# Optimization experiments

Hardware: AMD Instinct MI355X
Metric: run time of the kernel (lower is better)

## Reference

```python
import jax, jax.numpy as jnp
import numpy as np

G = 4096      # number of graphs in the batch
N = 524288    # total nodes across batch (avg 128 nodes/graph)
H = 128       # hidden_size


def setup_inputs() -> dict:
    key = jax.random.key(0)
    ks = jax.random.split(key, 8)
    s1 = 1.0 / np.sqrt(2 * H)
    s2 = 1.0 / np.sqrt(H)
    return {
        "updated_set": jax.random.normal(ks[0], (G, H), jnp.float32),
        "updated_node": jax.random.normal(ks[1], (N, H), jnp.float32),
        "segment_ids": jnp.sort(jax.random.randint(ks[2], (N,), 0, G, jnp.int32)),
        "Ws1": jax.random.normal(ks[3], (2 * H, H), jnp.float32) * s1,
        "bs1": jnp.zeros((H,), jnp.float32),
        "Ws2": jax.random.normal(ks[4], (H, H), jnp.float32) * s2,
        "bs2": jnp.zeros((H,), jnp.float32),
        "Wn1": jax.random.normal(ks[5], (2 * H, H), jnp.float32) * s1,
        "bn1": jnp.zeros((H,), jnp.float32),
        "Wn2": jax.random.normal(ks[6], (H, H), jnp.float32) * s2,
        "bn2": jnp.zeros((H,), jnp.float32),
    }


def reference(updated_set, updated_node, segment_ids, Ws1, bs1, Ws2, bs2, Wn1, bn1, Wn2, bn2):
    num_graphs = updated_set.shape[0]
    # SumPooling: segment-sum node features per graph -> [G, H]
    nodes_agg = jax.ops.segment_sum(updated_node, segment_ids, num_segments=num_graphs)
    # set update: concat([G,H],[G,H]) -> MLP 2H->H->H with ReLU
    s_in = jnp.concatenate([nodes_agg, updated_set], axis=1)
    s = jax.nn.relu(jax.nn.relu(s_in @ Ws1 + bs1) @ Ws2 + bs2)
    # tile(): broadcast each graph's set state to its nodes = gather by segment id
    n_in = jnp.concatenate([updated_node, s[segment_ids]], axis=1)  # [N, 2H]
    n = jax.nn.relu(jax.nn.relu(n_in @ Wn1 + bn1) @ Wn2 + bn2)
    return s, n
```

## Files before the change

### kernel.cpp

```cpp
#include <hip/hip_runtime.h>

#define NG 4096
#define NN 524288
#define H  128
#define H2 256

typedef __attribute__((ext_vector_type(8))) short bf16x8;
typedef __attribute__((ext_vector_type(4))) float floatx4;
typedef __attribute__((ext_vector_type(2))) unsigned int uint2v;

__device__ __forceinline__ unsigned short bf16r(float f) {
    unsigned int u = __builtin_bit_cast(unsigned int, f);
    u += 0x7fffu + ((u >> 16) & 1u);
    return (unsigned short)(u >> 16);
}
__device__ __forceinline__ unsigned int bf16pk2(float a, float b) {
    return (unsigned int)bf16r(a) | ((unsigned int)bf16r(b) << 16);
}
__device__ __forceinline__ bf16x8 pack8(floatx4 a, floatx4 b) {
    union { unsigned int u[4]; bf16x8 v; } r;
    r.u[0] = bf16pk2(a[0], a[1]);
    r.u[1] = bf16pk2(a[2], a[3]);
    r.u[2] = bf16pk2(b[0], b[1]);
    r.u[3] = bf16pk2(b[2], b[3]);
    return r.v;
}

__global__ __launch_bounds__(128) void seg_sum_kernel(
    const float* __restrict__ node, const int* __restrict__ seg,
    float* __restrict__ agg) {
    const int g = blockIdx.x;
    const int h = threadIdx.x;

    int lo = 0, hi = NN;
    while (lo < hi) { int mid = (lo + hi) >> 1; if (seg[mid] < g) lo = mid + 1; else hi = mid; }
    const int start = lo;
    hi = NN;
    while (lo < hi) { int mid = (lo + hi) >> 1; if (seg[mid] < g + 1) lo = mid + 1; else hi = mid; }
    const int end = lo;

    float a0 = 0.f, a1 = 0.f, a2 = 0.f, a3 = 0.f;
    int i = start;
    for (; i + 3 < end; i += 4) {
        a0 += node[(size_t)i * H + h];
        a1 += node[(size_t)(i + 1) * H + h];
        a2 += node[(size_t)(i + 2) * H + h];
        a3 += node[(size_t)(i + 3) * H + h];
    }
    for (; i < end; ++i) a0 += node[(size_t)i * H + h];
    agg[(size_t)g * H + h] = (a0 + a1) + (a2 + a3);
}

__global__ __launch_bounds__(128) void set_mlp_kernel(
    const float* __restrict__ agg, const float* __restrict__ uset,
    const float* __restrict__ Ws1, const float* __restrict__ bs1,
    const float* __restrict__ Ws2, const float* __restrict__ bs2,
    float* __restrict__ s_out) {
    __shared__ float sin[H2];
    __shared__ float h1[H];
    const int g = blockIdx.x;
    const int j = threadIdx.x;

    sin[j]     = agg[(size_t)g * H + j];
    sin[j + H] = uset[(size_t)g * H + j];
    __syncthreads();

    float acc = bs1[j];
    #pragma unroll 8
    for (int k = 0; k < H2; ++k)
        acc = fmaf(sin[k], Ws1[k * H + j], acc);
    h1[j] = fmaxf(acc, 0.f);
    __syncthreads();

    acc = bs2[j];
    #pragma unroll 8
    for (int k = 0; k < H; ++k)
        acc = fmaf(h1[k], Ws2[k * H + j], acc);
    s_out[(size_t)g * H + j] = fmaxf(acc, 0.f);
}

#define TILES 8

__global__ __launch_bounds__(256, 2) void node_mlp_mfma(
    const float* __restrict__ node, const int* __restrict__ seg,
    const float* __restrict__ s,
    const float* __restrict__ Wn1, const float* __restrict__ bn1,
    const float* __restrict__ Wn2, const float* __restrict__ bn2,
    float* __restrict__ n_out) {

    __shared__ unsigned short h1s[16 * 136];
    __shared__ float outs[16 * 132];

    const int tid   = threadIdx.x;
    const int wid   = tid >> 6;
    const int lane  = tid & 63;
    const int l16   = lane & 15;
    const int quad  = lane >> 4;
    const int fbase = wid * 32;

    bf16x8 A1[2][8];
    #pragma unroll
    for (int mt = 0; mt < 2; ++mt)
        #pragma unroll
        for (int kt = 0; kt < 8; ++kt) {
            const float* b = Wn1 + (size_t)(kt * 32 + quad * 8) * H
                                 + fbase + mt * 16 + l16;
            union { unsigned int u[4]; bf16x8 v; } r;
            #pragma unroll
            for (int j = 0; j < 4; ++j)
                r.u[j] = bf16pk2(b[(2 * j) * H], b[(2 * j + 1) * H]);
            A1[mt][kt] = r.v;
        }
    bf16x8 A2[2][4];
    #pragma unroll
    for (int mt = 0; mt < 2; ++mt)
        #pragma unroll
        for (int kt = 0; kt < 4; ++kt) {
            const float* b = Wn2 + (size_t)(kt * 32 + quad * 8) * H
                                 + fbase + mt * 16 + l16;
            union { unsigned int u[4]; bf16x8 v; } r;
            #pragma unroll
            for (int j = 0; j < 4; ++j)
                r.u[j] = bf16pk2(b[(2 * j) * H], b[(2 * j + 1) * H]);
            A2[mt][kt] = r.v;
        }
    floatx4 b1v[2], b2v[2];
    #pragma unroll
    for (int mt = 0; mt < 2; ++mt) {
        b1v[mt] = *(const floatx4*)(bn1 + fbase + mt * 16 + quad * 4);
        b2v[mt] = *(const floatx4*)(bn2 + fbase + mt * 16 + quad * 4);
    }

    const int nb0 = blockIdx.x * (TILES * 16);
    for (int t = 0; t < TILES; ++t) {
        const int nb  = nb0 + t * 16;
        const int row = nb + l16;
        const int sg  = seg[row];
        const float* nrow = node + (size_t)row * H;
        const float* srow = s    + (size_t)sg  * H;

        floatx4 acc1[2];
        acc1[0] = (floatx4){0.f, 0.f, 0.f, 0.f};
        acc1[1] = (floatx4){0.f, 0.f, 0.f, 0.f};
        #pragma unroll
        for (int kt = 0; kt < 8; ++kt) {
            const float* src = (kt < 4) ? (nrow + kt * 32 + quad * 8)
                                        : (srow + (kt - 4) * 32 + quad * 8);
            floatx4 f0 = *(const floatx4*)src;
            floatx4 f1 = *(const floatx4*)(src + 4);
            bf16x8 bf = pack8(f0, f1);
            acc1[0] = __builtin_amdgcn_mfma_f32_16x16x32_bf16(A1[0][kt], bf, acc1[0], 0, 0, 0);
            acc1[1] = __builtin_amdgcn_mfma_f32_16x16x32_bf16(A1[1][kt], bf, acc1[1], 0, 0, 0);
        }
        #pragma unroll
        for (int mt = 0; mt < 2; ++mt) {
            floatx4 v = acc1[mt] + b1v[mt];
            uint2v u;
            u[0] = bf16pk2(fmaxf(v[0], 0.f), fmaxf(v[1], 0.f));
            u[1] = bf16pk2(fmaxf(v[2], 0.f), fmaxf(v[3], 0.f));
            *(uint2v*)&h1s[l16 * 136 + fbase + mt * 16 + quad * 4] = u;
        }
        __syncthreads();

        floatx4 acc2[2];
        acc2[0] = (floatx4){0.f, 0.f, 0.f, 0.f};
        acc2[1] = (floatx4){0.f, 0.f, 0.f, 0.f};
        #pragma unroll
        for (int kt = 0; kt < 4; ++kt) {
            bf16x8 bf = *(const bf16x8*)&h1s[l16 * 136 + kt * 32 + quad * 8];
            acc2[0] = __builtin_amdgcn_mfma_f32_16x16x32_bf16(A2[0][kt], bf, acc2[0], 0, 0, 0);
            acc2[1] = __builtin_amdgcn_mfma_f32_16x16x32_bf16(A2[1][kt], bf, acc2[1], 0, 0, 0);
        }
        #pragma unroll
        for (int mt = 0; mt < 2; ++mt) {
            floatx4 v = acc2[mt] + b2v[mt];
            floatx4 o;
            o[0] = fmaxf(v[0], 0.f); o[1] = fmaxf(v[1], 0.f);
            o[2] = fmaxf(v[2], 0.f); o[3] = fmaxf(v[3], 0.f);
            *(floatx4*)&outs[l16 * 132 + fbase + mt * 16 + quad * 4] = o;
        }
        __syncthreads();

        {
            const int nidx = tid >> 4;
            const int col  = (tid & 15) * 8;
            floatx4 o0 = *(const floatx4*)&outs[nidx * 132 + col];
            floatx4 o1 = *(const floatx4*)&outs[nidx * 132 + col + 4];
            float* dst = n_out + (size_t)(nb + nidx) * H + col;
            *(floatx4*)dst       = o0;
            *(floatx4*)(dst + 4) = o1;
        }
        __syncthreads();
    }
}

extern "C" void kernel_launch(void* const* d_in, const int* in_sizes, int n_in,
                              void* d_out, int out_size, void* d_ws, size_t ws_size,
                              hipStream_t stream) {
    const float* updated_set  = (const float*)d_in[0];
    const float* updated_node = (const float*)d_in[1];
    const int*   segment_ids  = (const int*)  d_in[2];
    const float* Ws1 = (const float*)d_in[3];
    const float* bs1 = (const float*)d_in[4];
    const float* Ws2 = (const float*)d_in[5];
    const float* bs2 = (const float*)d_in[6];
    const float* Wn1 = (const float*)d_in[7];
    const float* bn1 = (const float*)d_in[8];
    const float* Wn2 = (const float*)d_in[9];
    const float* bn2 = (const float*)d_in[10];

    float* s_out = (float*)d_out;
    float* n_out = (float*)d_out + (size_t)NG * H;
    float* agg   = (float*)d_ws;

    seg_sum_kernel<<<NG, 128, 0, stream>>>(updated_node, segment_ids, agg);
    set_mlp_kernel<<<NG, 128, 0, stream>>>(agg, updated_set, Ws1, bs1, Ws2, bs2, s_out);
    node_mlp_mfma<<<NN / (TILES * 16), 256, 0, stream>>>(
        updated_node, segment_ids, s_out, Wn1, bn1, Wn2, bn2, n_out);
}
```

Measured before the change: 763.5 us.

## Use atomic chunked segment-sum, MFMA set MLP, and prefetch in node MLP

```diff
diff --git a/kernel.cpp b/kernel.cpp
--- a/kernel.cpp
+++ b/kernel.cpp
@@ -26,70 +26,51 @@
     return r.v;
 }
 
-__global__ __launch_bounds__(128) void seg_sum_kernel(
+#define SS_ROWS 256
+#define SS_SUB  4
+#define SS_LEN  (SS_ROWS / SS_SUB)
+
+__global__ __launch_bounds__(128) void seg_sum_atomic(
     const float* __restrict__ node, const int* __restrict__ seg,
     float* __restrict__ agg) {
-    const int g = blockIdx.x;
-    const int h = threadIdx.x;
-
-    int lo = 0, hi = NN;
-    while (lo < hi) { int mid = (lo + hi) >> 1; if (seg[mid] < g) lo = mid + 1; else hi = mid; }
-    const int start = lo;
-    hi = NN;
-    while (lo < hi) { int mid = (lo + hi) >> 1; if (seg[mid] < g + 1) lo = mid + 1; else hi = mid; }
-    const int end = lo;
-
-    float a0 = 0.f, a1 = 0.f, a2 = 0.f, a3 = 0.f;
-    int i = start;
-    for (; i + 3 < end; i += 4) {
-        a0 += node[(size_t)i * H + h];
-        a1 += node[(size_t)(i + 1) * H + h];
-        a2 += node[(size_t)(i + 2) * H + h];
-        a3 += node[(size_t)(i + 3) * H + h];
-    }
-    for (; i < end; ++i) a0 += node[(size_t)i * H + h];
-    agg[(size_t)g * H + h] = (a0 + a1) + (a2 + a3);
-}
-
-__global__ __launch_bounds__(128) void set_mlp_kernel(
-    const float* __restrict__ agg, const float* __restrict__ uset,
-    const float* __restrict__ Ws1, const float* __restrict__ bs1,
-    const float* __restrict__ Ws2, const float* __restrict__ bs2,
-    float* __restrict__ s_out) {
-    __shared__ float sin[H2];
-    __shared__ float h1[H];
-    const int g = blockIdx.x;
-    const int j = threadIdx.x;
-
-    sin[j]     = agg[(size_t)g * H + j];
-    sin[j + H] = uset[(size_t)g * H + j];
-    __syncthreads();
-
-    float acc = bs1[j];
-    #pragma unroll 8
-    for (int k = 0; k < H2; ++k)
-        acc = fmaf(sin[k], Ws1[k * H + j], acc);
-    h1[j] = fmaxf(acc, 0.f);
-    __syncthreads();
-
-    acc = bs2[j];
-    #pragma unroll 8
-    for (int k = 0; k < H; ++k)
-        acc = fmaf(h1[k], Ws2[k * H + j], acc);
-    s_out[(size_t)g * H + j] = fmaxf(acc, 0.f);
-}
-
-#define TILES 8
-
-__global__ __launch_bounds__(256, 2) void node_mlp_mfma(
-    const float* __restrict__ node, const int* __restrict__ seg,
-    const float* __restrict__ s,
-    const float* __restrict__ Wn1, const float* __restrict__ bn1,
-    const float* __restrict__ Wn2, const float* __restrict__ bn2,
-    float* __restrict__ n_out) {
-
-    __shared__ unsigned short h1s[16 * 136];
-    __shared__ float outs[16 * 132];
+    const int j    = threadIdx.x;
+    const int base = blockIdx.x * SS_ROWS;
+
+    float acc[SS_SUB];
+    int   cur[SS_SUB];
+    #pragma unroll
+    for (int c = 0; c < SS_SUB; ++c) {
+        cur[c] = seg[base + c * SS_LEN];
+        acc[c] = 0.f;
+    }
+    for (int r = 0; r < SS_LEN; ++r) {
+        #pragma unroll
+        for (int c = 0; c < SS_SUB; ++c) {
+            const int   row = base + c * SS_LEN + r;
+            const int   sgv = seg[row];
+            const float v   = node[(size_t)row * H + j];
+            if (sgv != cur[c]) {
+                atomicAdd(&agg[(size_t)cur[c] * H + j], acc[c]);
+                acc[c] = 0.f;
+                cur[c] = sgv;
+            }
+            acc[c] += v;
+        }
+    }
+    #pragma unroll
+    for (int c = 0; c < SS_SUB; ++c)
+        atomicAdd(&agg[(size_t)cur[c] * H + j], acc[c]);
+}
+
+template<int TILES_, bool GATHER, bool NT>
+__global__ __launch_bounds__(256) void mlp_mfma(
+    const float* __restrict__ in0, const int* __restrict__ seg,
+    const float* __restrict__ in1,
+    const float* __restrict__ W1, const float* __restrict__ b1,
+    const float* __restrict__ W2, const float* __restrict__ b2,
+    float* __restrict__ outp) {
+
+    __shared__ unsigned short h1s[2][16 * 136];
 
     const int tid   = threadIdx.x;
     const int wid   = tid >> 6;
@@ -103,8 +84,8 @@
     for (int mt = 0; mt < 2; ++mt)
         #pragma unroll
         for (int kt = 0; kt < 8; ++kt) {
-            const float* b = Wn1 + (size_t)(kt * 32 + quad * 8) * H
-                                 + fbase + mt * 16 + l16;
+            const float* b = W1 + (size_t)(kt * 32 + quad * 8) * H
+                                + fbase + mt * 16 + l16;
             union { unsigned int u[4]; bf16x8 v; } r;
             #pragma unroll
             for (int j = 0; j < 4; ++j)
@@ -116,8 +97,8 @@
     for (int mt = 0; mt < 2; ++mt)
         #pragma unroll
         for (int kt = 0; kt < 4; ++kt) {
-            const float* b = Wn2 + (size_t)(kt * 32 + quad * 8) * H
-                                 + fbase + mt * 16 + l16;
+            const float* b = W2 + (size_t)(kt * 32 + quad * 8) * H
+                                + fbase + mt * 16 + l16;
             union { unsigned int u[4]; bf16x8 v; } r;
             #pragma unroll
             for (int j = 0; j < 4; ++j)
@@ -127,27 +108,42 @@
     floatx4 b1v[2], b2v[2];
     #pragma unroll
     for (int mt = 0; mt < 2; ++mt) {
-        b1v[mt] = *(const floatx4*)(bn1 + fbase + mt * 16 + quad * 4);
-        b2v[mt] = *(const floatx4*)(bn2 + fbase + mt * 16 + quad * 4);
-    }
-
-    const int nb0 = blockIdx.x * (TILES * 16);
-    for (int t = 0; t < TILES; ++t) {
-        const int nb  = nb0 + t * 16;
-        const int row = nb + l16;
-        const int sg  = seg[row];
-        const float* nrow = node + (size_t)row * H;
-        const float* srow = s    + (size_t)sg  * H;
+        b1v[mt] = *(const floatx4*)(b1 + fbase + mt * 16 + quad * 4);
+        b2v[mt] = *(const floatx4*)(b2 + fbase + mt * 16 + quad * 4);
+    }
+
+    const int nb0 = blockIdx.x * (TILES_ * 16);
+
+    int sg;
+    floatx4 pf[8];
+    {
+        const int row = nb0 + l16;
+        sg = GATHER ? seg[row] : row;
+        const float* p = in0 + (size_t)row * H;
+        #pragma unroll
+        for (int i = 0; i < 4; ++i) {
+            pf[2 * i]     = *(const floatx4*)(p + i * 32 + quad * 8);
+            pf[2 * i + 1] = *(const floatx4*)(p + i * 32 + quad * 8 + 4);
+        }
+    }
+
+    for (int t = 0; t < TILES_; ++t) {
+        const int nb = nb0 + t * 16;
+        const float* srow = in1 + (size_t)sg * H;
 
         floatx4 acc1[2];
         acc1[0] = (floatx4){0.f, 0.f, 0.f, 0.f};
         acc1[1] = (floatx4){0.f, 0.f, 0.f, 0.f};
         #pragma unroll
-        for (int kt = 0; kt < 8; ++kt) {
-            const float* src = (kt < 4) ? (nrow + kt * 32 + quad * 8)
-                                        : (srow + (kt - 4) * 32 + quad * 8);
-            floatx4 f0 = *(const floatx4*)src;
-            floatx4 f1 = *(const floatx4*)(src + 4);
+        for (int kt = 0; kt < 4; ++kt) {
+            bf16x8 bf = pack8(pf[2 * kt], pf[2 * kt + 1]);
+            acc1[0] = __builtin_amdgcn_mfma_f32_16x16x32_bf16(A1[0][kt], bf, acc1[0], 0, 0, 0);
+            acc1[1] = __builtin_amdgcn_mfma_f32_16x16x32_bf16(A1[1][kt], bf, acc1[1], 0, 0, 0);
+        }
+        #pragma unroll
+        for (int kt = 4; kt < 8; ++kt) {
+            floatx4 f0 = *(const floatx4*)(srow + (kt - 4) * 32 + quad * 8);
+            floatx4 f1 = *(const floatx4*)(srow + (kt - 4) * 32 + quad * 8 + 4);
             bf16x8 bf = pack8(f0, f1);
             acc1[0] = __builtin_amdgcn_mfma_f32_16x16x32_bf16(A1[0][kt], bf, acc1[0], 0, 0, 0);
             acc1[1] = __builtin_amdgcn_mfma_f32_16x16x32_bf16(A1[1][kt], bf, acc1[1], 0, 0, 0);
@@ -158,8 +154,20 @@
             uint2v u;
             u[0] = bf16pk2(fmaxf(v[0], 0.f), fmaxf(v[1], 0.f));
             u[1] = bf16pk2(fmaxf(v[2], 0.f), fmaxf(v[3], 0.f));
-            *(uint2v*)&h1s[l16 * 136 + fbase + mt * 16 + quad * 4] = u;
-        }
+            *(uint2v*)&h1s[t & 1][l16 * 136 + fbase + mt * 16 + quad * 4] = u;
+        }
+
+        if (t + 1 < TILES_) {
+            const int row = nb + 16 + l16;
+            sg = GATHER ? seg[row] : row;
+            const float* p = in0 + (size_t)row * H;
+            #pragma unroll
+            for (int i = 0; i < 4; ++i) {
+                pf[2 * i]     = *(const floatx4*)(p + i * 32 + quad * 8);
+                pf[2 * i + 1] = *(const floatx4*)(p + i * 32 + quad * 8 + 4);
+            }
+        }
+
         __syncthreads();
 
         floatx4 acc2[2];
@@ -167,7 +175,7 @@
         acc2[1] = (floatx4){0.f, 0.f, 0.f, 0.f};
         #pragma unroll
         for (int kt = 0; kt < 4; ++kt) {
-            bf16x8 bf = *(const bf16x8*)&h1s[l16 * 136 + kt * 32 + quad * 8];
+            bf16x8 bf = *(const bf16x8*)&h1s[t & 1][l16 * 136 + kt * 32 + quad * 8];
             acc2[0] = __builtin_amdgcn_mfma_f32_16x16x32_bf16(A2[0][kt], bf, acc2[0], 0, 0, 0);
             acc2[1] = __builtin_amdgcn_mfma_f32_16x16x32_bf16(A2[1][kt], bf, acc2[1], 0, 0, 0);
         }
@@ -177,20 +185,10 @@
             floatx4 o;
             o[0] = fmaxf(v[0], 0.f); o[1] = fmaxf(v[1], 0.f);
             o[2] = fmaxf(v[2], 0.f); o[3] = fmaxf(v[3], 0.f);
-            *(floatx4*)&outs[l16 * 132 + fbase + mt * 16 + quad * 4] = o;
-        }
-        __syncthreads();
-
-        {
-            const int nidx = tid >> 4;
-            const int col  = (tid & 15) * 8;
-            floatx4 o0 = *(const floatx4*)&outs[nidx * 132 + col];
-            floatx4 o1 = *(const floatx4*)&outs[nidx * 132 + col + 4];
-            float* dst = n_out + (size_t)(nb + nidx) * H + col;
-            *(floatx4*)dst       = o0;
-            *(floatx4*)(dst + 4) = o1;
-        }
-        __syncthreads();
+            float* dst = outp + (size_t)(nb + l16) * H + fbase + mt * 16 + quad * 4;
+            if (NT) __builtin_nontemporal_store(o, (floatx4*)dst);
+            else    *(floatx4*)dst = o;
+        }
     }
 }
 
@@ -213,8 +211,13 @@
     float* n_out = (float*)d_out + (size_t)NG * H;
     float* agg   = (float*)d_ws;
 
-    seg_sum_kernel<<<NG, 128, 0, stream>>>(updated_node, segment_ids, agg);
-    set_mlp_kernel<<<NG, 128, 0, stream>>>(agg, updated_set, Ws1, bs1, Ws2, bs2, s_out);
-    node_mlp_mfma<<<NN / (TILES * 16), 256, 0, stream>>>(
+    hipMemsetAsync(agg, 0, (size_t)NG * H * sizeof(float), stream);
+
+    seg_sum_atomic<<<NN / SS_ROWS, 128, 0, stream>>>(updated_node, segment_ids, agg);
+
+    mlp_mfma<1, false, false><<<NG / 16, 256, 0, stream>>>(
+        agg, nullptr, updated_set, Ws1, bs1, Ws2, bs2, s_out);
+
+    mlp_mfma<8, true, true><<<NN / (8 * 16), 256, 0, stream>>>(
         updated_node, segment_ids, s_out, Wn1, bn1, Wn2, bn2, n_out);
 }
```

Measured after the change: 686.1 us. -10.1%, faster.
